# Optimization experiments

Measured on AMD Instinct MI355X. Metric: run time of the kernel, lower is better.

The kernel has to match this reference:

```python
import jax, jax.numpy as jnp
import numpy as np

EPS = 1e-12  # F.normalize eps


def _gather_nb(var, idx):
    # var: [B, N, C], idx: [B, N, K] -> [B, N, K, C]; out[b,n,k,c] = var[b, idx[b,n,k], c]
    return jnp.take_along_axis(var[:, :, None, :], idx[:, :, :, None], axis=1)


def _l2norm(v):
    n = jnp.sqrt(jnp.sum(v * v, axis=-1, keepdims=True))
    return v / jnp.maximum(n, EPS)


def setup_inputs() -> dict:
    key = jax.random.key(0)
    ks = jax.random.split(key, 16)
    B, N, K, dim, hid = 4, 4096, 16, 128, 64
    s = 0.05
    return {
        "pos": jax.random.normal(ks[0], (B, N, 3), jnp.float32),
        "x": jax.random.normal(ks[1], (B, dim, N), jnp.float32),
        "idx": jax.random.randint(ks[2], (B, N, K), 0, N, jnp.int64),
        "dist": jax.random.uniform(ks[3], (B, N, K), jnp.float32),
        "W_qkv": jax.random.normal(ks[4], (3 * dim, dim), jnp.float32) * s,
        "W1": jax.random.normal(ks[5], (hid, 10), jnp.float32) * s,
        "b1": jax.random.normal(ks[6], (hid,), jnp.float32) * s,
        "W2": jax.random.normal(ks[7], (dim, hid), jnp.float32) * s,
        "b2": jax.random.normal(ks[8], (dim,), jnp.float32) * s,
        "Wm1": jax.random.normal(ks[9], (4 * dim, dim), jnp.float32) * s,
        "bm1": jax.random.normal(ks[10], (4 * dim,), jnp.float32) * s,
        "Wm2": jax.random.normal(ks[11], (dim, 4 * dim), jnp.float32) * s,
        "bm2": jax.random.normal(ks[12], (dim,), jnp.float32) * s,
    }


def reference(pos, x, idx, dist, W_qkv, W1, b1, W2, b2, Wm1, bm1, Wm2, bm2):
    B, _, N = x.shape
    xt = jnp.transpose(x, (0, 2, 1))                      # [B, N, C]
    qkv = xt @ W_qkv.T                                    # [B, N, 3C]
    Q, K_, V = jnp.split(qkv, 3, axis=-1)

    Qg = _gather_nb(Q, idx)                               # [B, N, K, C]
    Kg = _gather_nb(K_, idx)
    Vg = _gather_nb(V, idx)

    # position embedding: [center(3) | neighbor(3) | diff(3) | dist(1)] -> MLP 10->hid->C
    pos_nb = _gather_nb(pos, idx)                         # [B, N, K, 3]
    pos_c = jnp.broadcast_to(pos[:, :, None, :], pos_nb.shape)
    feat10 = jnp.concatenate(
        [pos_c, pos_nb, pos_c - pos_nb, dist[..., None]], axis=-1)  # [B, N, K, 10]
    pos_emb = jax.nn.relu(feat10 @ W1.T + b1) @ W2.T + b2  # [B, N, K, C]

    Knorm = _l2norm(Kg + pos_emb)                         # [B, N, K, C]
    Vrel = jax.nn.relu(Vg + pos_emb)                      # [B, N, K, C]
    Qn = _l2norm(Qg)                                      # [B, N, K, C]

    # kv_context: contract over N per neighbor slot k -> [B, K, C, C]
    kv = jnp.einsum('bnkc,bnkd->bkcd', Knorm, Vrel)
    # (1/N) Qn @ kv, then sum over k -> [B, N, C]
    agg = jnp.einsum('bnkc,bkcd->bnd', Qn, kv) / N

    out = jax.nn.relu(agg @ Wm1.T + bm1) @ Wm2.T + bm2 + xt  # [B, N, C]
    return jnp.transpose(out, (0, 2, 1))                     # [B, C, N]
```

## Files before the change

### kernel.cpp

```cpp
#include <hip/hip_runtime.h>
#include <math.h>

#define Bn 4
#define Nn 4096
#define Kn 16
#define Cn 128
#define HIDn 64

#define OFF_WQKVBF 0
#define OFF_WM1BF  24576
#define OFF_WM2BF  57344
#define OFF_W2BFG  90112
#define OFF_QNBF   95232
#define OFF_KMBF   1143808
#define OFF_VMBF   2192384
#define OFF_KVT32  3240960
#define OFF_KVTBF  4289536
#define OFF_AGG0   4813824
#define OFF_AGG1   6910976
#define OFF_FLAG   9008128

typedef short bf16x8 __attribute__((ext_vector_type(8)));
typedef float f32x4 __attribute__((ext_vector_type(4)));

__device__ inline unsigned short f2bf(float f) {
  union { float f; unsigned u; } v; v.f = f;
  unsigned r = v.u + 0x7fffu + ((v.u >> 16) & 1u);
  return (unsigned short)(r >> 16);
}
__device__ inline float b2f(unsigned short s) {
  union { unsigned u; float f; } v; v.u = ((unsigned)s) << 16; return v.f;
}

__global__ void k0_prep(const float* __restrict__ Wqkv,
                        const float* __restrict__ Wm1, const float* __restrict__ Wm2,
                        const float* __restrict__ W2,
                        const int* __restrict__ idx_raw, float* ws) {
  if (blockIdx.x == 0 && threadIdx.x == 0) {
    int any = 0;
    for (int i = 0; i < 64; ++i) any |= idx_raw[2 * i + 1];
    ((int*)(ws + OFF_FLAG))[0] = (any == 0) ? 1 : 0;
  }
  int t = blockIdx.x * 256 + threadIdx.x;
  if (t < 49152) { ((unsigned short*)(ws + OFF_WQKVBF))[t] = f2bf(Wqkv[t]); return; }
  t -= 49152;
  if (t < 65536) { ((unsigned short*)(ws + OFF_WM1BF))[t] = f2bf(Wm1[t]); return; }
  t -= 65536;
  if (t < 65536) { ((unsigned short*)(ws + OFF_WM2BF))[t] = f2bf(Wm2[t]); return; }
  t -= 65536;
  if (t < 8192) { ((unsigned short*)(ws + OFF_W2BFG))[t] = f2bf(W2[t]); return; }
}

__global__ __launch_bounds__(256, 2) void k1_qkv(const float* __restrict__ x, float* ws) {
  __shared__ __align__(16) unsigned short a_lds[32 * 136];
  __shared__ __align__(16) float qkv_lds[32 * 388];
  const unsigned short* Wq = (const unsigned short*)(ws + OFF_WQKVBF);
  unsigned short* Qnbf = (unsigned short*)(ws + OFF_QNBF);
  unsigned short* KmBF = (unsigned short*)(ws + OFF_KMBF);
  unsigned short* VmBF = (unsigned short*)(ws + OFF_VMBF);
  int b = blockIdx.x >> 7;
  int n0 = (blockIdx.x & 127) << 5;
  int t = threadIdx.x;
  int w = t >> 6, l = t & 63, ml = l & 15, gq = l >> 4;
#pragma unroll
  for (int i = 0; i < 16; ++i) {
    int id = t + 256 * i;
    int c = id >> 5, j = id & 31;
    a_lds[j * 136 + c] = f2bf(x[(b * Cn + c) * Nn + n0 + j]);
  }
  __syncthreads();
  f32x4 acc[2][6];
#pragma unroll
  for (int i = 0; i < 2; ++i)
#pragma unroll
    for (int j = 0; j < 6; ++j) acc[i][j] = (f32x4)0.f;
#pragma unroll
  for (int kc = 0; kc < 4; ++kc) {
    bf16x8 av0 = *(const bf16x8*)&a_lds[ml * 136 + kc * 32 + 8 * gq];
    bf16x8 av1 = *(const bf16x8*)&a_lds[(ml + 16) * 136 + kc * 32 + 8 * gq];
#pragma unroll
    for (int nf = 0; nf < 6; ++nf) {
      int m = 96 * w + 16 * nf + ml;
      bf16x8 bv = *(const bf16x8*)&Wq[m * 128 + kc * 32 + 8 * gq];
      acc[0][nf] = __builtin_amdgcn_mfma_f32_16x16x32_bf16(av0, bv, acc[0][nf], 0, 0, 0);
      acc[1][nf] = __builtin_amdgcn_mfma_f32_16x16x32_bf16(av1, bv, acc[1][nf], 0, 0, 0);
    }
  }
#pragma unroll
  for (int mf = 0; mf < 2; ++mf)
#pragma unroll
    for (int nf = 0; nf < 6; ++nf)
#pragma unroll
      for (int r = 0; r < 4; ++r)
        qkv_lds[(16 * mf + 4 * gq + r) * 388 + 96 * w + 16 * nf + ml] = acc[mf][nf][r];
  __syncthreads();
  {
    int g = t >> 3, l8 = t & 7;
    float4 q4[4];
    float ss = 0.f;
#pragma unroll
    for (int q = 0; q < 4; ++q) {
      q4[q] = *(const float4*)&qkv_lds[g * 388 + l8 * 16 + 4 * q];
      ss = fmaf(q4[q].x, q4[q].x, ss); ss = fmaf(q4[q].y, q4[q].y, ss);
      ss = fmaf(q4[q].z, q4[q].z, ss); ss = fmaf(q4[q].w, q4[q].w, ss);
    }
    ss += __shfl_xor(ss, 1); ss += __shfl_xor(ss, 2); ss += __shfl_xor(ss, 4);
    float sc = 1.f / fmaxf(sqrtf(ss), 1e-12f);
    union { unsigned short us[8]; uint4 u4; } o0, o1;
#pragma unroll
    for (int q = 0; q < 2; ++q) {
      o0.us[q * 4 + 0] = f2bf(q4[q].x * sc); o0.us[q * 4 + 1] = f2bf(q4[q].y * sc);
      o0.us[q * 4 + 2] = f2bf(q4[q].z * sc); o0.us[q * 4 + 3] = f2bf(q4[q].w * sc);
    }
#pragma unroll
    for (int q = 0; q < 2; ++q) {
      o1.us[q * 4 + 0] = f2bf(q4[2 + q].x * sc); o1.us[q * 4 + 1] = f2bf(q4[2 + q].y * sc);
      o1.us[q * 4 + 2] = f2bf(q4[2 + q].z * sc); o1.us[q * 4 + 3] = f2bf(q4[2 + q].w * sc);
    }
    *(uint4*)&Qnbf[(b * Nn + n0 + g) * Cn + l8 * 16] = o0.u4;
    *(uint4*)&Qnbf[(b * Nn + n0 + g) * Cn + l8 * 16 + 8] = o1.u4;
  }
#pragma unroll
  for (int i = 0; i < 2; ++i) {
    int id = t + 256 * i;
    int row = id >> 4, c8 = id & 15;
    const float* kp = &qkv_lds[row * 388 + 128 + c8 * 8];
    const float* vp = &qkv_lds[row * 388 + 256 + c8 * 8];
    union { unsigned short us[8]; uint4 u4; } ko, vo;
#pragma unroll
    for (int j = 0; j < 8; ++j) { ko.us[j] = f2bf(kp[j]); vo.us[j] = f2bf(vp[j]); }
    *(uint4*)&KmBF[(b * Nn + n0 + row) * Cn + c8 * 8] = ko.u4;
    *(uint4*)&VmBF[(b * Nn + n0 + row) * Cn + c8 * 8] = vo.u4;
  }
}

#define CH2 8
__global__ __launch_bounds__(256, 2) void k2_kv(const float* __restrict__ pos,
                                                const float* __restrict__ dist,
                                                const int* __restrict__ idxp,
                                                const float* __restrict__ W1,
                                                const float* __restrict__ b1,
                                                const float* __restrict__ b2,
                                                float* ws) {
  __shared__ __align__(16) unsigned short h_lds[32 * 72];
  __shared__ __align__(16) float pe_lds[32 * 132];
  __shared__ __align__(16) unsigned short KnT[2][128 * 40];
  __shared__ __align__(16) unsigned short VrT[2][128 * 40];

  const unsigned short* KmBF = (const unsigned short*)(ws + OFF_KMBF);
  const unsigned short* VmBF = (const unsigned short*)(ws + OFF_VMBF);
  const unsigned short* W2g = (const unsigned short*)(ws + OFF_W2BFG);
  float* kvt = ws + OFF_KVT32;
  int flag = ((const int*)(ws + OFF_FLAG))[0];

  int bid = blockIdx.x;
  int b = bid & 3;
  int rest = bid >> 2;
  int k = rest & 15, ch = rest >> 4;
  int t = threadIdx.x;
  int w = t >> 6, l = t & 63;
  int ml = l & 15, gq = l >> 4;

  int g = t >> 3, l8 = t & 7;
  int nl = (t >> 3) & 7, half = t & 7;
  int n_b2 = 8 * w + nl;
  int swb = ((w ^ (half & 3)) << 3) + nl;

  float b2v0 = b2[32 * w + ml];
  float b2v1 = b2[32 * w + 16 + ml];

  f32x4 acc[2][8];
#pragma unroll
  for (int i = 0; i < 2; ++i)
#pragma unroll
    for (int j = 0; j < 8; ++j) acc[i][j] = (f32x4)0.f;

  int nbase = ch * 512;
  union U8 { unsigned short us[8]; uint4 u4; };

  int fidx_m = (b * Nn + nbase + g) * Kn + k;
  int jn_m = flag ? idxp[2 * fidx_m] : idxp[fidx_m];
  float dd = dist[fidx_m];
  float pc0 = pos[(b * Nn + nbase + g) * 3 + 0];
  float pc1 = pos[(b * Nn + nbase + g) * 3 + 1];
  float pc2 = pos[(b * Nn + nbase + g) * 3 + 2];
  float pn0 = pos[(b * Nn + jn_m) * 3 + 0];
  float pn1 = pos[(b * Nn + jn_m) * 3 + 1];
  float pn2 = pos[(b * Nn + jn_m) * 3 + 2];
  int fidx_b = (b * Nn + nbase + n_b2) * Kn + k;
  int jn_b = flag ? idxp[2 * fidx_b] : idxp[fidx_b];
  U8 ka, kb, va, vb;
  {
    const unsigned short* krow = &KmBF[(b * Nn + jn_b) * Cn];
    const unsigned short* vrow = &VmBF[(b * Nn + jn_b) * Cn];
    ka.u4 = *(const uint4*)&krow[half * 16];
    kb.u4 = *(const uint4*)&krow[half * 16 + 8];
    va.u4 = *(const uint4*)&vrow[half * 16];
    vb.u4 = *(const uint4*)&vrow[half * 16 + 8];
  }

  for (int it = 0; it < 16; ++it) {
    {
      float f10[10] = {pc0, pc1, pc2, pn0, pn1, pn2, pc0 - pn0, pc1 - pn1, pc2 - pn2, dd};
      union { unsigned short us[8]; uint4 u4; } hv;
#pragma unroll
      for (int oo = 0; oo < 8; ++oo) {
        int o = l8 * 8 + oo;
        float a = b1[o];
#pragma unroll
        for (int i2 = 0; i2 < 10; ++i2) a = fmaf(W1[o * 10 + i2], f10[i2], a);
        hv.us[oo] = f2bf(fmaxf(a, 0.f));
      }
      *(uint4*)&h_lds[g * 72 + l8 * 8] = hv.u4;
    }
    int itn = (it < 15) ? it + 1 : 15;
    int n0n = nbase + itn * 32;
    int fidx_mn = (b * Nn + n0n + g) * Kn + k;
    int jn_mn = flag ? idxp[2 * fidx_mn] : idxp[fidx_mn];
    float ddn = dist[fidx_mn];
    int fidx_bn = (b * Nn + n0n + n_b2) * Kn + k;
    int jn_bn = flag ? idxp[2 * fidx_bn] : idxp[fidx_bn];
    __syncthreads();
    if (it > 0) {
      const unsigned short* ktp = KnT[(it - 1) & 1];
      const unsigned short* vtp = VrT[(it - 1) & 1];
      bf16x8 av[2];
#pragma unroll
      for (int mf = 0; mf < 2; ++mf) {
        int d = 32 * w + 16 * mf + ml;
        int blk = gq ^ ((2 * w + mf) & 3);
        av[mf] = *(const bf16x8*)&vtp[d * 40 + 8 * blk];
      }
#pragma unroll
      for (int nf = 0; nf < 8; ++nf) {
        int c = 16 * nf + ml;
        int blk = gq ^ (nf & 3);
        bf16x8 bv = *(const bf16x8*)&ktp[c * 40 + 8 * blk];
#pragma unroll
        for (int mf = 0; mf < 2; ++mf)
          acc[mf][nf] = __builtin_amdgcn_mfma_f32_16x16x32_bf16(av[mf], bv, acc[mf][nf], 0, 0, 0);
      }
    }
    {
      f32x4 pacc[2][2];
#pragma unroll
      for (int i = 0; i < 2; ++i)
#pragma unroll
        for (int j = 0; j < 2; ++j) pacc[i][j] = (f32x4)0.f;
#pragma unroll
      for (int hc = 0; hc < 64; hc += 32) {
        bf16x8 av[2];
#pragma unroll
        for (int mf = 0; mf < 2; ++mf)
          av[mf] = *(const bf16x8*)&h_lds[(ml + 16 * mf) * 72 + hc + 8 * gq];
#pragma unroll
        for (int nf = 0; nf < 2; ++nf) {
          int c = 32 * w + 16 * nf + ml;
          bf16x8 bv = *(const bf16x8*)&W2g[c * 64 + hc + 8 * gq];
          pacc[0][nf] = __builtin_amdgcn_mfma_f32_16x16x32_bf16(av[0], bv, pacc[0][nf], 0, 0, 0);
          pacc[1][nf] = __builtin_amdgcn_mfma_f32_16x16x32_bf16(av[1], bv, pacc[1][nf], 0, 0, 0);
        }
      }
#pragma unroll
      for (int mf = 0; mf < 2; ++mf)
#pragma unroll
        for (int nf = 0; nf < 2; ++nf) {
          int c = 32 * w + 16 * nf + ml;
          float bias = nf ? b2v1 : b2v0;
#pragma unroll
          for (int r = 0; r < 4; ++r)
            pe_lds[(16 * mf + 4 * gq + r) * 132 + c] = pacc[mf][nf][r] + bias;
        }
    }
    __syncthreads();
    {
      float p[16];
#pragma unroll
      for (int q = 0; q < 4; ++q) {
        float4 p4 = *(const float4*)&pe_lds[n_b2 * 132 + half * 16 + 4 * q];
        p[4 * q] = p4.x; p[4 * q + 1] = p4.y; p[4 * q + 2] = p4.z; p[4 * q + 3] = p4.w;
      }
      unsigned short* kdst = KnT[it & 1];
      unsigned short* vdst = VrT[it & 1];
      float kr[16];
      float ss = 0.f;
#pragma unroll
      for (int j = 0; j < 16; ++j) {
        float kg = b2f((j < 8) ? ka.us[j] : kb.us[j - 8]);
        float vg = b2f((j < 8) ? va.us[j] : vb.us[j - 8]);
        kr[j] = kg + p[j];
        float vv = fmaxf(vg + p[j], 0.f);
        ss = fmaf(kr[j], kr[j], ss);
        vdst[(half * 16 + j) * 40 + swb] = f2bf(vv);
      }
      ss += __shfl_xor(ss, 1); ss += __shfl_xor(ss, 2); ss += __shfl_xor(ss, 4);
      float sc = 1.f / fmaxf(sqrtf(ss), 1e-12f);
#pragma unroll
      for (int j = 0; j < 16; ++j)
        kdst[(half * 16 + j) * 40 + swb] = f2bf(kr[j] * sc);
    }
    float pc0n = pos[(b * Nn + n0n + g) * 3 + 0];
    float pc1n = pos[(b * Nn + n0n + g) * 3 + 1];
    float pc2n = pos[(b * Nn + n0n + g) * 3 + 2];
    float pn0n = pos[(b * Nn + jn_mn) * 3 + 0];
    float pn1n = pos[(b * Nn + jn_mn) * 3 + 1];
    float pn2n = pos[(b * Nn + jn_mn) * 3 + 2];
    U8 kan, kbn, van, vbn;
    {
      const unsigned short* krow = &KmBF[(b * Nn + jn_bn) * Cn];
      const unsigned short* vrow = &VmBF[(b * Nn + jn_bn) * Cn];
      kan.u4 = *(const uint4*)&krow[half * 16];
      kbn.u4 = *(const uint4*)&krow[half * 16 + 8];
      van.u4 = *(const uint4*)&vrow[half * 16];
      vbn.u4 = *(const uint4*)&vrow[half * 16 + 8];
    }
    dd = ddn;
    pc0 = pc0n; pc1 = pc1n; pc2 = pc2n;
    pn0 = pn0n; pn1 = pn1n; pn2 = pn2n;
    ka.u4 = kan.u4; kb.u4 = kbn.u4; va.u4 = van.u4; vb.u4 = vbn.u4;
  }
  __syncthreads();
  {
    const unsigned short* ktp = KnT[15 & 1];
    const unsigned short* vtp = VrT[15 & 1];
    bf16x8 av[2];
#pragma unroll
    for (int mf = 0; mf < 2; ++mf) {
      int d = 32 * w + 16 * mf + ml;
      int blk = gq ^ ((2 * w + mf) & 3);
      av[mf] = *(const bf16x8*)&vtp[d * 40 + 8 * blk];
    }
#pragma unroll
    for (int nf = 0; nf < 8; ++nf) {
      int c = 16 * nf + ml;
      int blk = gq ^ (nf & 3);
      bf16x8 bv = *(const bf16x8*)&ktp[c * 40 + 8 * blk];
#pragma unroll
      for (int mf = 0; mf < 2; ++mf)
        acc[mf][nf] = __builtin_amdgcn_mfma_f32_16x16x32_bf16(av[mf], bv, acc[mf][nf], 0, 0, 0);
    }
  }
  float* kvp = kvt + (b * Kn + k) * Cn * Cn;
#pragma unroll
  for (int mf = 0; mf < 2; ++mf)
#pragma unroll
    for (int nf = 0; nf < 8; ++nf) {
      int c = 16 * nf + ml;
#pragma unroll
      for (int r = 0; r < 4; ++r) {
        int d = 32 * w + 16 * mf + 4 * gq + r;
        atomicAdd(&kvp[d * Cn + c], acc[mf][nf][r]);
      }
    }
}

__global__ __launch_bounds__(256) void k2b_cvt(float* ws) {
  const float* src = ws + OFF_KVT32;
  unsigned short* dst = (unsigned short*)(ws + OFF_KVTBF);
  int i = blockIdx.x * 256 + threadIdx.x;
  float4 a = *(const float4*)&src[i * 8];
  float4 c = *(const float4*)&src[i * 8 + 4];
  union { unsigned short us[8]; uint4 u4; } o;
  o.us[0] = f2bf(a.x); o.us[1] = f2bf(a.y); o.us[2] = f2bf(a.z); o.us[3] = f2bf(a.w);
  o.us[4] = f2bf(c.x); o.us[5] = f2bf(c.y); o.us[6] = f2bf(c.z); o.us[7] = f2bf(c.w);
  *(uint4*)&dst[i * 8] = o.u4;
}

__global__ __launch_bounds__(256, 4) void k3_agg(const int* __restrict__ idxp, float* ws) {
  __shared__ __align__(16) unsigned short qt[32 * 136];
  const unsigned short* Qnbf = (const unsigned short*)(ws + OFF_QNBF);
  const unsigned short* kvtbf = (const unsigned short*)(ws + OFF_KVTBF);
  int flag = ((const int*)(ws + OFF_FLAG))[0];

  int bid = blockIdx.x;
  int b = bid & 3;
  int kh = (bid >> 2) & 1;
  int nt = bid >> 3;
  int n0 = nt * 32;
  int t = threadIdx.x;
  int w = t >> 6, l = t & 63;
  int ml = l & 15, gq = l >> 4;

  f32x4 acc[2][2];
#pragma unroll
  for (int i = 0; i < 2; ++i)
#pragma unroll
    for (int j = 0; j < 2; ++j) acc[i][j] = (f32x4)0.f;

  for (int kk = 0; kk < 8; ++kk) {
    int k = kh * 8 + kk;
    __syncthreads();
#pragma unroll
    for (int i = 0; i < 2; ++i) {
      int id = t + 256 * i;
      int row = id >> 4, c16 = id & 15;
      int fidx = (b * Nn + n0 + row) * Kn + k;
      int jn = flag ? idxp[2 * fidx] : idxp[fidx];
      uint4 v = *(const uint4*)&Qnbf[(b * Nn + jn) * Cn + c16 * 8];
      *(uint4*)&qt[row * 136 + c16 * 8] = v;
    }
    __syncthreads();
    const unsigned short* kvp = &kvtbf[(b * Kn + k) * Cn * Cn];
#pragma unroll
    for (int c0 = 0; c0 < 128; c0 += 32) {
      bf16x8 a0 = *(const bf16x8*)&qt[ml * 136 + c0 + 8 * gq];
      bf16x8 a1 = *(const bf16x8*)&qt[(ml + 16) * 136 + c0 + 8 * gq];
#pragma unroll
      for (int nf = 0; nf < 2; ++nf) {
        int d = 32 * w + 16 * nf + ml;
        bf16x8 bv = *(const bf16x8*)&kvp[d * Cn + c0 + 8 * gq];
        acc[0][nf] = __builtin_amdgcn_mfma_f32_16x16x32_bf16(a0, bv, acc[0][nf], 0, 0, 0);
        acc[1][nf] = __builtin_amdgcn_mfma_f32_16x16x32_bf16(a1, bv, acc[1][nf], 0, 0, 0);
      }
    }
  }
  float* ag = ws + (kh ? OFF_AGG1 : OFF_AGG0);
#pragma unroll
  for (int mf = 0; mf < 2; ++mf)
#pragma unroll
    for (int nf = 0; nf < 2; ++nf) {
      int d = 32 * w + 16 * nf + ml;
#pragma unroll
      for (int r = 0; r < 4; ++r) {
        int n = n0 + 16 * mf + 4 * gq + r;
        ag[(b * Nn + n) * Cn + d] = acc[mf][nf][r];
      }
    }
}

__global__ __launch_bounds__(256, 2) void k4_mlp(const float* __restrict__ x,
                                                 const float* __restrict__ bm1,
                                                 const float* __restrict__ bm2,
                                                 float* __restrict__ out, float* ws) {
  __shared__ __align__(16) unsigned short a_lds[32 * 136];
  __shared__ __align__(16) unsigned short h_lds[32 * 520];
  __shared__ float out_s[128 * 33];
  const float* agg0 = ws + OFF_AGG0;
  const float* agg1 = ws + OFF_AGG1;
  const unsigned short* Wm1bf = (const unsigned short*)(ws + OFF_WM1BF);
  const unsigned short* Wm2bf = (const unsigned short*)(ws + OFF_WM2BF);
  const float invN = 1.f / (float)Nn;
  int b = blockIdx.x >> 7;
  int n0 = (blockIdx.x & 127) << 5;
  int t = threadIdx.x;
  int w = t >> 6, l = t & 63, ml = l & 15, gq = l >> 4;
#pragma unroll
  for (int i = 0; i < 4; ++i) {
    int id = t + 256 * i;
    int row = id >> 5, c4 = id & 31;
    int off = (b * Nn + n0 + row) * Cn + c4 * 4;
    float4 v0 = *(const float4*)&agg0[off];
    float4 v1 = *(const float4*)&agg1[off];
    union { unsigned short us[4]; uint2 u2; } o;
    o.us[0] = f2bf((v0.x + v1.x) * invN); o.us[1] = f2bf((v0.y + v1.y) * invN);
    o.us[2] = f2bf((v0.z + v1.z) * invN); o.us[3] = f2bf((v0.w + v1.w) * invN);
    *(uint2*)&a_lds[row * 136 + c4 * 4] = o.u2;
  }
  __syncthreads();
  {
    f32x4 hacc[2][8];
#pragma unroll
    for (int i = 0; i < 2; ++i)
#pragma unroll
      for (int j = 0; j < 8; ++j) hacc[i][j] = (f32x4)0.f;
#pragma unroll
    for (int kc = 0; kc < 4; ++kc) {
      bf16x8 av0 = *(const bf16x8*)&a_lds[ml * 136 + kc * 32 + 8 * gq];
      bf16x8 av1 = *(const bf16x8*)&a_lds[(ml + 16) * 136 + kc * 32 + 8 * gq];
#pragma unroll
      for (int nf = 0; nf < 8; ++nf) {
        int h = 128 * w + 16 * nf + ml;
        bf16x8 bv = *(const bf16x8*)&Wm1bf[h * 128 + kc * 32 + 8 * gq];
        hacc[0][nf] = __builtin_amdgcn_mfma_f32_16x16x32_bf16(av0, bv, hacc[0][nf], 0, 0, 0);
        hacc[1][nf] = __builtin_amdgcn_mfma_f32_16x16x32_bf16(av1, bv, hacc[1][nf], 0, 0, 0);
      }
    }
#pragma unroll
    for (int mf = 0; mf < 2; ++mf)
#pragma unroll
      for (int nf = 0; nf < 8; ++nf) {
        int h = 128 * w + 16 * nf + ml;
        float bias = bm1[h];
#pragma unroll
        for (int r = 0; r < 4; ++r)
          h_lds[(16 * mf + 4 * gq + r) * 520 + h] = f2bf(fmaxf(hacc[mf][nf][r] + bias, 0.f));
      }
  }
  __syncthreads();
  {
    f32x4 oacc[2][2];
#pragma unroll
    for (int i = 0; i < 2; ++i)
#pragma unroll
      for (int j = 0; j < 2; ++j) oacc[i][j] = (f32x4)0.f;
#pragma unroll
    for (int kc = 0; kc < 16; ++kc) {
      bf16x8 av0 = *(const bf16x8*)&h_lds[ml * 520 + kc * 32 + 8 * gq];
      bf16x8 av1 = *(const bf16x8*)&h_lds[(ml + 16) * 520 + kc * 32 + 8 * gq];
#pragma unroll
      for (int nf = 0; nf < 2; ++nf) {
        int co = 32 * w + 16 * nf + ml;
        bf16x8 bv = *(const bf16x8*)&Wm2bf[co * 512 + kc * 32 + 8 * gq];
        oacc[0][nf] = __builtin_amdgcn_mfma_f32_16x16x32_bf16(av0, bv, oacc[0][nf], 0, 0, 0);
        oacc[1][nf] = __builtin_amdgcn_mfma_f32_16x16x32_bf16(av1, bv, oacc[1][nf], 0, 0, 0);
      }
    }
#pragma unroll
    for (int mf = 0; mf < 2; ++mf)
#pragma unroll
      for (int nf = 0; nf < 2; ++nf) {
        int co = 32 * w + 16 * nf + ml;
        float bias = bm2[co];
#pragma unroll
        for (int r = 0; r < 4; ++r)
          out_s[co * 33 + 16 * mf + 4 * gq + r] = oacc[mf][nf][r] + bias;
      }
  }
  __syncthreads();
#pragma unroll
  for (int i = 0; i < 16; ++i) {
    int id = t + 256 * i;
    int co = id >> 5, j = id & 31;
    out[(b * Cn + co) * Nn + n0 + j] = out_s[co * 33 + j] + x[(b * Cn + co) * Nn + n0 + j];
  }
}

extern "C" void kernel_launch(void* const* d_in, const int* in_sizes, int n_in,
                              void* d_out, int out_size, void* d_ws, size_t ws_size,
                              hipStream_t stream) {
  const float* pos  = (const float*)d_in[0];
  const float* x    = (const float*)d_in[1];
  const int*   idx  = (const int*)d_in[2];
  const float* dist = (const float*)d_in[3];
  const float* Wqkv = (const float*)d_in[4];
  const float* W1   = (const float*)d_in[5];
  const float* b1   = (const float*)d_in[6];
  const float* W2   = (const float*)d_in[7];
  const float* b2   = (const float*)d_in[8];
  const float* Wm1  = (const float*)d_in[9];
  const float* bm1  = (const float*)d_in[10];
  const float* Wm2  = (const float*)d_in[11];
  const float* bm2  = (const float*)d_in[12];
  float* out = (float*)d_out;
  float* ws = (float*)d_ws;

  hipMemsetAsync(ws + OFF_KVT32, 0, (size_t)Bn * Kn * Cn * Cn * sizeof(float), stream);
  hipLaunchKernelGGL(k0_prep, dim3(736), dim3(256), 0, stream, Wqkv, Wm1, Wm2, W2, idx, ws);
  hipLaunchKernelGGL(k1_qkv, dim3(Bn * 128), dim3(256), 0, stream, x, ws);
  hipLaunchKernelGGL(k2_kv, dim3(Bn * Kn * CH2), dim3(256), 0, stream, pos, dist, idx, W1, b1, b2, ws);
  hipLaunchKernelGGL(k2b_cvt, dim3(512), dim3(256), 0, stream, ws);
  hipLaunchKernelGGL(k3_agg, dim3(Bn * 2 * 128), dim3(256), 0, stream, idx, ws);
  hipLaunchKernelGGL(k4_mlp, dim3(Bn * 128), dim3(256), 0, stream, x, bm1, bm2, out, ws);
}
```

Before: 152.6 us.

## Shrink k2_kv LDS and split N finer to raise occupancy

```diff
diff --git a/kernel.cpp b/kernel.cpp
--- a/kernel.cpp
+++ b/kernel.cpp
@@ -134,8 +134,8 @@
   }
 }
 
-#define CH2 8
-__global__ __launch_bounds__(256, 2) void k2_kv(const float* __restrict__ pos,
+#define CH2 16
+__global__ __launch_bounds__(256, 4) void k2_kv(const float* __restrict__ pos,
                                                 const float* __restrict__ dist,
                                                 const int* __restrict__ idxp,
                                                 const float* __restrict__ W1,
@@ -143,9 +143,9 @@
                                                 const float* __restrict__ b2,
                                                 float* ws) {
   __shared__ __align__(16) unsigned short h_lds[32 * 72];
-  __shared__ __align__(16) float pe_lds[32 * 132];
-  __shared__ __align__(16) unsigned short KnT[2][128 * 40];
-  __shared__ __align__(16) unsigned short VrT[2][128 * 40];
+  __shared__ __align__(16) unsigned short pe_bf[32 * 136];
+  __shared__ __align__(16) unsigned short KnT[128 * 40];
+  __shared__ __align__(16) unsigned short VrT[128 * 40];
 
   const unsigned short* KmBF = (const unsigned short*)(ws + OFF_KMBF);
   const unsigned short* VmBF = (const unsigned short*)(ws + OFF_VMBF);
@@ -175,7 +175,7 @@
 #pragma unroll
     for (int j = 0; j < 8; ++j) acc[i][j] = (f32x4)0.f;
 
-  int nbase = ch * 512;
+  int nbase = ch * 256;
   union U8 { unsigned short us[8]; uint4 u4; };
 
   int fidx_m = (b * Nn + nbase + g) * Kn + k;
@@ -199,7 +199,7 @@
     vb.u4 = *(const uint4*)&vrow[half * 16 + 8];
   }
 
-  for (int it = 0; it < 16; ++it) {
+  for (int it = 0; it < 8; ++it) {
     {
       float f10[10] = {pc0, pc1, pc2, pn0, pn1, pn2, pc0 - pn0, pc1 - pn1, pc2 - pn2, dd};
       union { unsigned short us[8]; uint4 u4; } hv;
@@ -213,7 +213,7 @@
       }
       *(uint4*)&h_lds[g * 72 + l8 * 8] = hv.u4;
     }
-    int itn = (it < 15) ? it + 1 : 15;
+    int itn = (it < 7) ? it + 1 : 7;
     int n0n = nbase + itn * 32;
     int fidx_mn = (b * Nn + n0n + g) * Kn + k;
     int jn_mn = flag ? idxp[2 * fidx_mn] : idxp[fidx_mn];
@@ -221,26 +221,6 @@
     int fidx_bn = (b * Nn + n0n + n_b2) * Kn + k;
     int jn_bn = flag ? idxp[2 * fidx_bn] : idxp[fidx_bn];
     __syncthreads();
-    if (it > 0) {
-      const unsigned short* ktp = KnT[(it - 1) & 1];
-      const unsigned short* vtp = VrT[(it - 1) & 1];
-      bf16x8 av[2];
-#pragma unroll
-      for (int mf = 0; mf < 2; ++mf) {
-        int d = 32 * w + 16 * mf + ml;
-        int blk = gq ^ ((2 * w + mf) & 3);
-        av[mf] = *(const bf16x8*)&vtp[d * 40 + 8 * blk];
-      }
-#pragma unroll
-      for (int nf = 0; nf < 8; ++nf) {
-        int c = 16 * nf + ml;
-        int blk = gq ^ (nf & 3);
-        bf16x8 bv = *(const bf16x8*)&ktp[c * 40 + 8 * blk];
-#pragma unroll
-        for (int mf = 0; mf < 2; ++mf)
-          acc[mf][nf] = __builtin_amdgcn_mfma_f32_16x16x32_bf16(av[mf], bv, acc[mf][nf], 0, 0, 0);
-      }
-    }
     {
       f32x4 pacc[2][2];
 #pragma unroll
@@ -269,35 +249,31 @@
           float bias = nf ? b2v1 : b2v0;
 #pragma unroll
           for (int r = 0; r < 4; ++r)
-            pe_lds[(16 * mf + 4 * gq + r) * 132 + c] = pacc[mf][nf][r] + bias;
+            pe_bf[(16 * mf + 4 * gq + r) * 136 + c] = f2bf(pacc[mf][nf][r] + bias);
         }
     }
     __syncthreads();
     {
-      float p[16];
-#pragma unroll
-      for (int q = 0; q < 4; ++q) {
-        float4 p4 = *(const float4*)&pe_lds[n_b2 * 132 + half * 16 + 4 * q];
-        p[4 * q] = p4.x; p[4 * q + 1] = p4.y; p[4 * q + 2] = p4.z; p[4 * q + 3] = p4.w;
-      }
-      unsigned short* kdst = KnT[it & 1];
-      unsigned short* vdst = VrT[it & 1];
+      U8 pa, pb;
+      pa.u4 = *(const uint4*)&pe_bf[n_b2 * 136 + half * 16];
+      pb.u4 = *(const uint4*)&pe_bf[n_b2 * 136 + half * 16 + 8];
       float kr[16];
       float ss = 0.f;
 #pragma unroll
       for (int j = 0; j < 16; ++j) {
+        float pe = b2f((j < 8) ? pa.us[j] : pb.us[j - 8]);
         float kg = b2f((j < 8) ? ka.us[j] : kb.us[j - 8]);
         float vg = b2f((j < 8) ? va.us[j] : vb.us[j - 8]);
-        kr[j] = kg + p[j];
-        float vv = fmaxf(vg + p[j], 0.f);
+        kr[j] = kg + pe;
+        float vv = fmaxf(vg + pe, 0.f);
         ss = fmaf(kr[j], kr[j], ss);
-        vdst[(half * 16 + j) * 40 + swb] = f2bf(vv);
+        VrT[(half * 16 + j) * 40 + swb] = f2bf(vv);
       }
       ss += __shfl_xor(ss, 1); ss += __shfl_xor(ss, 2); ss += __shfl_xor(ss, 4);
       float sc = 1.f / fmaxf(sqrtf(ss), 1e-12f);
 #pragma unroll
       for (int j = 0; j < 16; ++j)
-        kdst[(half * 16 + j) * 40 + swb] = f2bf(kr[j] * sc);
+        KnT[(half * 16 + j) * 40 + swb] = f2bf(kr[j] * sc);
     }
     float pc0n = pos[(b * Nn + n0n + g) * 3 + 0];
     float pc1n = pos[(b * Nn + n0n + g) * 3 + 1];
@@ -314,31 +290,29 @@
       van.u4 = *(const uint4*)&vrow[half * 16];
       vbn.u4 = *(const uint4*)&vrow[half * 16 + 8];
     }
+    __syncthreads();
+    {
+      bf16x8 av[2];
+#pragma unroll
+      for (int mf = 0; mf < 2; ++mf) {
+        int d = 32 * w + 16 * mf + ml;
+        int blk = gq ^ ((2 * w + mf) & 3);
+        av[mf] = *(const bf16x8*)&VrT[d * 40 + 8 * blk];
+      }
+#pragma unroll
+      for (int nf = 0; nf < 8; ++nf) {
+        int c = 16 * nf + ml;
+        int blk = gq ^ (nf & 3);
+        bf16x8 bv = *(const bf16x8*)&KnT[c * 40 + 8 * blk];
+#pragma unroll
+        for (int mf = 0; mf < 2; ++mf)
+          acc[mf][nf] = __builtin_amdgcn_mfma_f32_16x16x32_bf16(av[mf], bv, acc[mf][nf], 0, 0, 0);
+      }
+    }
     dd = ddn;
     pc0 = pc0n; pc1 = pc1n; pc2 = pc2n;
     pn0 = pn0n; pn1 = pn1n; pn2 = pn2n;
     ka.u4 = kan.u4; kb.u4 = kbn.u4; va.u4 = van.u4; vb.u4 = vbn.u4;
-  }
-  __syncthreads();
-  {
-    const unsigned short* ktp = KnT[15 & 1];
-    const unsigned short* vtp = VrT[15 & 1];
-    bf16x8 av[2];
-#pragma unroll
-    for (int mf = 0; mf < 2; ++mf) {
-      int d = 32 * w + 16 * mf + ml;
-      int blk = gq ^ ((2 * w + mf) & 3);
-      av[mf] = *(const bf16x8*)&vtp[d * 40 + 8 * blk];
-    }
-#pragma unroll
-    for (int nf = 0; nf < 8; ++nf) {
-      int c = 16 * nf + ml;
-      int blk = gq ^ (nf & 3);
-      bf16x8 bv = *(const bf16x8*)&ktp[c * 40 + 8 * blk];
-#pragma unroll
-      for (int mf = 0; mf < 2; ++mf)
-        acc[mf][nf] = __builtin_amdgcn_mfma_f32_16x16x32_bf16(av[mf], bv, acc[mf][nf], 0, 0, 0);
-    }
   }
   float* kvp = kvt + (b * Kn + k) * Cn * Cn;
 #pragma unroll
```

Measured after the change: 299.8 us. 1.96x slower.
